# Performance work log

Hardware: AMD Instinct MI355X
Metric: run time of the kernel (lower is better)

Reference implementation:

```python
import jax, jax.numpy as jnp
import numpy as np

B, N, E = 4, 25000, 1600000
NODE_DIM, EMBED = 64, 64
NUM = B * N


def setup_inputs() -> dict:
    key = jax.random.key(0)
    ks = jax.random.split(key, 12)
    p = lambda k, s: jax.random.normal(k, s, jnp.float32) * 0.05
    z = lambda s: jnp.zeros(s, jnp.float32)
    return {
        "node_feat": jax.random.normal(ks[0], (B, N, NODE_DIM), jnp.float32),
        "src": jax.random.randint(ks[1], (E,), 0, NUM),
        "dst": jax.random.randint(ks[2], (E,), 0, NUM),
        "edge_weight": jax.random.uniform(ks[3], (E,), jnp.float32),
        "h": z((NUM, EMBED)),
        "W_cz": p(ks[4], (NODE_DIM, EMBED)), "b_cz": z((EMBED,)),
        "W_cr": p(ks[5], (NODE_DIM, EMBED)), "b_cr": z((EMBED,)),
        "W_ch": p(ks[6], (NODE_DIM, EMBED)), "b_ch": z((EMBED,)),
        "W_lz": p(ks[7], (2 * EMBED, EMBED)), "b_lz": z((EMBED,)),
        "W_lr": p(ks[8], (2 * EMBED, EMBED)), "b_lr": z((EMBED,)),
        "W_lh": p(ks[9], (2 * EMBED, EMBED)), "b_lh": z((EMBED,)),
        "W_head": p(ks[10], (EMBED, 1)), "b_head": z((1,)),
    }


def gcn_conv(x, W, b, src, dst, ew):
    # PyG GCNConv: self-loops (fill=1) + symmetric normalization, then linear.
    n = x.shape[0]
    loop = jnp.arange(n)
    s = jnp.concatenate([src, loop])
    d = jnp.concatenate([dst, loop])
    w = jnp.concatenate([ew, jnp.ones((n,), x.dtype)])
    deg = jax.ops.segment_sum(w, d, num_segments=n)
    dinv = jnp.where(deg > 0, jax.lax.rsqrt(deg), 0.0)
    norm = dinv[s] * w * dinv[d]                      # [E+n]
    xw = x @ W                                        # [n, EMBED]
    out = jax.ops.segment_sum(xw[s] * norm[:, None], d, num_segments=n)
    return out + b


def tgcn_cell(x, h, src, dst, ew,
              W_cz, b_cz, W_cr, b_cr, W_ch, b_ch,
              W_lz, b_lz, W_lr, b_lr, W_lh, b_lh):
    Z = jax.nn.sigmoid(
        jnp.concatenate([gcn_conv(x, W_cz, b_cz, src, dst, ew), h], axis=1) @ W_lz + b_lz)
    R = jax.nn.sigmoid(
        jnp.concatenate([gcn_conv(x, W_cr, b_cr, src, dst, ew), h], axis=1) @ W_lr + b_lr)
    H_tilde = jnp.tanh(
        jnp.concatenate([gcn_conv(x, W_ch, b_ch, src, dst, ew), h * R], axis=1) @ W_lh + b_lh)
    return Z * h + (1.0 - Z) * H_tilde


def reference(node_feat, src, dst, edge_weight, h,
              W_cz, b_cz, W_cr, b_cr, W_ch, b_ch,
              W_lz, b_lz, W_lr, b_lr, W_lh, b_lh,
              W_head, b_head):
    Bv, Nv, _ = node_feat.shape
    x = node_feat.reshape(Bv * Nv, -1)
    h0 = tgcn_cell(x, h, src, dst, edge_weight,
                   W_cz, b_cz, W_cr, b_cr, W_ch, b_ch,
                   W_lz, b_lz, W_lr, b_lr, W_lh, b_lh)
    z = jax.nn.relu(h0)
    z = (z @ W_head + b_head).reshape(Bv, Nv, -1)
    return (z, h0)
```

## Files before the change

kernel.cpp:

```cpp
#include <hip/hip_runtime.h>
#include <hip/hip_fp16.h>
#include <stdint.h>

typedef unsigned long long u64;
typedef _Float16 half8 __attribute__((ext_vector_type(8)));
typedef float f32x4 __attribute__((ext_vector_type(4)));

#define EPB 6144
#define CAPC 5440

__device__ __forceinline__ float sigm(float x) { return 1.0f / (1.0f + __expf(-x)); }
__device__ __forceinline__ float tanhfast(float x) { return 1.0f - 2.0f / (__expf(2.0f * x) + 1.0f); }
__device__ __forceinline__ int rli(int v, int k) { return __builtin_amdgcn_readlane(v, k); }
__device__ __forceinline__ float rlf(float v, int k) {
    return __int_as_float(__builtin_amdgcn_readlane(__float_as_int(v), k));
}

__global__ void k_pre(const float* __restrict__ Wcz, const float* __restrict__ bcz,
                      const float* __restrict__ Wcr, const float* __restrict__ bcr,
                      const float* __restrict__ Wch, const float* __restrict__ bch,
                      const float* __restrict__ Wlz, const float* __restrict__ blz,
                      const float* __restrict__ Wlr, const float* __restrict__ blr,
                      const float* __restrict__ Wlh, const float* __restrict__ blh,
                      const float4* __restrict__ h4, __half* __restrict__ aggh,
                      __half* __restrict__ B1f, __half* __restrict__ B2f,
                      float* __restrict__ bias, int* __restrict__ cursor, int hq) {
    int bid = blockIdx.x;
    if (bid < 113) {
        int tid = bid * 256 + threadIdx.x;
        if (tid < 1024) cursor[tid] = 0;
        if (tid < 24576) {
            int k = tid / 192, nc = tid % 192;
            int g = nc >> 6, j = nc & 63;
            const float* Wc = (g == 0) ? Wcz : (g == 1) ? Wcr : Wch;
            const float* Wl = (g == 0) ? Wlz : (g == 1) ? Wlr : Wlh;
            float v;
            if (k < 64) {
                float acc = 0.f;
                for (int m = 0; m < 64; m++) acc += Wc[k * 64 + m] * Wl[m * 64 + j];
                v = acc;
            } else {
                v = (g < 2) ? Wl[k * 64 + j] : 0.f;
            }
            int kt = k >> 5, nt = nc >> 4;
            int lane = (((k >> 3) & 3) << 4) | (nc & 15);
            B1f[(((kt * 12 + nt) * 64 + lane) << 3) + (k & 7)] = (__half)v;
        } else if (tid < 24576 + 4096) {
            int t = tid - 24576;
            int k = t >> 6, nc = t & 63;
            float v = Wlh[(64 + k) * 64 + nc];
            int kt = k >> 5, nt = nc >> 4;
            int lane = (((k >> 3) & 3) << 4) | (nc & 15);
            B2f[(((kt * 4 + nt) * 64 + lane) << 3) + (k & 7)] = (__half)v;
        } else if (tid < 24576 + 4096 + 192) {
            int t = tid - 24576 - 4096;
            int g = t >> 6, j = t & 63;
            const float* bc = (g == 0) ? bcz : (g == 1) ? bcr : bch;
            const float* Wl = (g == 0) ? Wlz : (g == 1) ? Wlr : Wlh;
            const float* bl = (g == 0) ? blz : (g == 1) ? blr : blh;
            float acc = bl[j];
            for (int m = 0; m < 64; m++) acc += bc[m] * Wl[m * 64 + j];
            bias[t] = acc;
        }
    } else {
        int i = (bid - 113) * 256 + threadIdx.x;
        if (i < hq) {
            float4 hv = h4[i];
            int elem = i * 4;
            int node = elem >> 6, c = elem & 63;
            __half2* ho = (__half2*)(aggh + (((size_t)node) << 7) + 64 + c);
            ho[0] = __floats2half2_rn(hv.x, hv.y);
            ho[1] = __floats2half2_rn(hv.z, hv.w);
        }
    }
}

__global__ void __launch_bounds__(1024) k_bin(const int* __restrict__ src, const int* __restrict__ dst,
                                              const float* __restrict__ ew,
                                              int* __restrict__ cursor, u64* __restrict__ binned,
                                              int E, int R) {
    __shared__ u64 recs[EPB];
    __shared__ int hist[512];
    __shared__ int loff[512];
    __shared__ int curL[512];
    __shared__ int gbase[512];

    int tid = threadIdx.x;
    if (tid < 512) hist[tid] = 0;
    __syncthreads();

    int base = blockIdx.x * EPB;
    int cntE = min(EPB, E - base);

    u64 myrec[6];
    int myr[6];
#pragma unroll
    for (int j = 0; j < 6; j++) {
        int idx = tid + j * 1024;
        if (idx < cntE) {
            int e = base + idx;
            int d = dst[e], s = src[e];
            float w = ew[e];
            int r = d >> 8;
            myr[j] = r;
            myrec[j] = (u64)((unsigned)s | ((unsigned)(d & 255) << 17)) | ((u64)__float_as_uint(w) << 32);
            atomicAdd(&hist[r], 1);
        } else myr[j] = -1;
    }
    __syncthreads();

    if (tid < 64) {
        int sums[8], tot = 0;
#pragma unroll
        for (int q = 0; q < 8; q++) { sums[q] = hist[tid * 8 + q]; tot += sums[q]; }
        int scan = tot;
#pragma unroll
        for (int o = 1; o < 64; o <<= 1) {
            int v = __shfl_up(scan, o);
            if (tid >= o) scan += v;
        }
        int run = scan - tot;
#pragma unroll
        for (int q = 0; q < 8; q++) { loff[tid * 8 + q] = run; run += sums[q]; }
    }
    if (tid < 512) curL[tid] = 0;
    if (tid < R) {
        int hcnt = hist[tid];
        if (hcnt > 0) gbase[tid] = tid * CAPC + atomicAdd(&cursor[tid], hcnt);
    }
    __syncthreads();

#pragma unroll
    for (int j = 0; j < 6; j++) {
        if (myr[j] >= 0) {
            int p = atomicAdd(&curL[myr[j]], 1);
            recs[loff[myr[j]] + p] = myrec[j];
        }
    }
    __syncthreads();

    int wave = tid >> 6, lane = tid & 63;
    for (int r = wave; r < R; r += 16) {
        int len = hist[r];
        if (!len) continue;
        int gb = gbase[r], lo = loff[r];
        int capEnd = (r + 1) * CAPC;
        for (int i = lane; i < len; i += 64)
            if (gb + i < capEnd) binned[(size_t)(gb + i)] = recs[lo + i];
    }
}

__global__ void __launch_bounds__(1024) k_sort(const int* __restrict__ cursor,
                                               u64* __restrict__ binned,
                                               const float2* __restrict__ x2,
                                               float* __restrict__ dinv,
                                               __half2* __restrict__ xs2,
                                               int* __restrict__ off_g, int* __restrict__ len_g,
                                               int n) {
    __shared__ u64 srt[CAPC];
    __shared__ int hist[256];
    __shared__ int noff[256];
    __shared__ int cur[256];
    __shared__ float degw[256];

    int r = blockIdx.x, tid = threadIdx.x;
    if (tid < 256) { hist[tid] = 0; degw[tid] = 0.f; }
    __syncthreads();

    int cnt = min(cursor[r], CAPC);
    u64* B = binned + (size_t)r * CAPC;

    for (int i = tid; i < cnt; i += 1024) {
        u64 m = B[i];
        int dl = ((unsigned)m >> 17) & 255;
        atomicAdd(&hist[dl], 1);
        atomicAdd(&degw[dl], __uint_as_float((unsigned)(m >> 32)));
    }
    __syncthreads();

    if (tid < 64) {
        int s0 = hist[tid * 4], s1 = hist[tid * 4 + 1], s2 = hist[tid * 4 + 2], s3 = hist[tid * 4 + 3];
        int tot = s0 + s1 + s2 + s3;
        int scan = tot;
#pragma unroll
        for (int o = 1; o < 64; o <<= 1) {
            int v = __shfl_up(scan, o);
            if (tid >= o) scan += v;
        }
        int run = scan - tot;
        noff[tid * 4] = run; run += s0;
        noff[tid * 4 + 1] = run; run += s1;
        noff[tid * 4 + 2] = run; run += s2;
        noff[tid * 4 + 3] = run;
    }
    __syncthreads();

    if (tid < 256) {
        int node = r * 256 + tid;
        float dv = rsqrtf(1.0f + degw[tid]);
        if (node < n) {
            dinv[node] = dv;
            off_g[node] = r * CAPC + noff[tid];
            len_g[node] = hist[tid];
        }
        cur[tid] = noff[tid];
        degw[tid] = dv;
    }
    __syncthreads();

    for (int i = tid; i < cnt; i += 1024) {
        u64 m = B[i];
        int dl = ((unsigned)m >> 17) & 255;
        int p = atomicAdd(&cur[dl], 1);
        srt[p] = (u64)((unsigned)m & 0x1FFFF) | (m & 0xFFFFFFFF00000000ULL);
    }
    __syncthreads();

    for (int i = tid; i < cnt; i += 1024) B[i] = srt[i];
    int nbase = r * 256;
    for (int i = tid; i < 256 * 32; i += 1024) {
        int nl = i >> 5, cp = i & 31;
        int node = nbase + nl;
        if (node < n) {
            float2 xv = x2[((size_t)node << 5) + cp];
            float dv = degw[nl];
            xs2[((size_t)node << 5) + cp] = __floats2half2_rn(dv * xv.x, dv * xv.y);
        }
    }
}

__global__ void __launch_bounds__(256) k_gather(const int* __restrict__ off_g, const int* __restrict__ len_g,
                                                const u64* __restrict__ csr, const float* __restrict__ dinv,
                                                const __half* __restrict__ xs,
                                                __half* __restrict__ aggh, int n) {
    int lane = threadIdx.x & 63;
    int wid = __builtin_amdgcn_readfirstlane(threadIdx.x >> 6);
    int d = blockIdx.x * 4 + wid;
    if (d >= n) return;
    int o0 = off_g[d], L = len_g[d];
    float dd = dinv[d];
    float acc[16];
#pragma unroll
    for (int j = 0; j < 16; j++) acc[j] = 0.f;
    acc[0] = (float)xs[((size_t)d << 6) + lane];

    for (int base = 0; base < L; base += 64) {
        int c = min(64, L - base);
        u64 m = (lane < c) ? csr[(size_t)(o0 + base) + lane] : 0;
        int s_l = (unsigned)m & 0x1FFFF;
        float w_l = __uint_as_float((unsigned)(m >> 32));
        int k = 0;
        for (; k + 16 <= c; k += 16) {
            int ss[16]; float ww[16], xr[16];
#pragma unroll
            for (int j = 0; j < 16; j++) { ss[j] = rli(s_l, k + j); ww[j] = rlf(w_l, k + j); }
#pragma unroll
            for (int j = 0; j < 16; j++) xr[j] = (float)xs[((size_t)ss[j] << 6) + lane];
#pragma unroll
            for (int j = 0; j < 16; j++) acc[j] = fmaf(ww[j], xr[j], acc[j]);
        }
        for (; k + 4 <= c; k += 4) {
            int ss[4]; float ww[4], xr[4];
#pragma unroll
            for (int j = 0; j < 4; j++) { ss[j] = rli(s_l, k + j); ww[j] = rlf(w_l, k + j); }
#pragma unroll
            for (int j = 0; j < 4; j++) xr[j] = (float)xs[((size_t)ss[j] << 6) + lane];
#pragma unroll
            for (int j = 0; j < 4; j++) acc[j] = fmaf(ww[j], xr[j], acc[j]);
        }
        for (; k < c; k++) {
            int s0 = rli(s_l, k);
            float w0 = rlf(w_l, k);
            acc[0] = fmaf(w0, (float)xs[((size_t)s0 << 6) + lane], acc[0]);
        }
    }
    float s = ((acc[0] + acc[1]) + (acc[2] + acc[3])) + ((acc[4] + acc[5]) + (acc[6] + acc[7]))
            + ((acc[8] + acc[9]) + (acc[10] + acc[11])) + ((acc[12] + acc[13]) + (acc[14] + acc[15]));
    aggh[((size_t)d << 7) + lane] = (__half)(dd * s);
}

__global__ void __launch_bounds__(256, 2) k_node(
        const __half* __restrict__ aggh,
        const __half* __restrict__ B1f_g, const __half* __restrict__ B2f_g,
        const float* __restrict__ bias_g, const float* __restrict__ Whead,
        const float* __restrict__ bhead,
        float* __restrict__ out_head, float* __restrict__ out_h, int n) {

    __shared__ __half B1s[24576];
    __shared__ __half B2s[4096];
    __shared__ float biasS[192];
    __shared__ float whS[64];
    __shared__ __half hrb[4][16 * 72];

    int tid = threadIdx.x;
    {
        const uint4* s1 = (const uint4*)B1f_g; uint4* d1 = (uint4*)B1s;
        for (int i = tid; i < 3072; i += 256) d1[i] = s1[i];
        const uint4* s2 = (const uint4*)B2f_g; uint4* d2 = (uint4*)B2s;
        for (int i = tid; i < 512; i += 256) d2[i] = s2[i];
        if (tid < 192) biasS[tid] = bias_g[tid];
        if (tid < 64) whS[tid] = Whead[tid];
    }
    __syncthreads();

    int lane = tid & 63;
    int wave = tid >> 6;
    int quad = lane >> 4;
    int l15 = lane & 15;

    float bz4[4], br4[4], bh4[4], wh4[4];
#pragma unroll
    for (int nt = 0; nt < 4; nt++) {
        bz4[nt] = biasS[nt * 16 + l15];
        br4[nt] = biasS[64 + nt * 16 + l15];
        bh4[nt] = biasS[128 + nt * 16 + l15];
        wh4[nt] = whS[nt * 16 + l15];
    }
    float bhv = bhead[0];
    __half* myhr = &hrb[wave][0];
    const half8* B1v = (const half8*)B1s;
    const half8* B2v = (const half8*)B2s;

    int mbase = blockIdx.x * 64 + wave * 16;
    if (mbase < n) {
        const half8* arow = (const half8*)(aggh + (((size_t)(mbase + l15)) << 7) + (quad << 3));
        half8 a0 = arow[0], a1 = arow[4], a2 = arow[8], a3 = arow[12];

        f32x4 acc[12];
#pragma unroll
        for (int nt = 0; nt < 12; nt++) acc[nt] = (f32x4){0.f, 0.f, 0.f, 0.f};

#pragma unroll
        for (int nt = 0; nt < 12; nt++) {
            acc[nt] = __builtin_amdgcn_mfma_f32_16x16x32_f16(a0, B1v[(0 * 12 + nt) * 64 + lane], acc[nt], 0, 0, 0);
            acc[nt] = __builtin_amdgcn_mfma_f32_16x16x32_f16(a1, B1v[(1 * 12 + nt) * 64 + lane], acc[nt], 0, 0, 0);
            acc[nt] = __builtin_amdgcn_mfma_f32_16x16x32_f16(a2, B1v[(2 * 12 + nt) * 64 + lane], acc[nt], 0, 0, 0);
            acc[nt] = __builtin_amdgcn_mfma_f32_16x16x32_f16(a3, B1v[(3 * 12 + nt) * 64 + lane], acc[nt], 0, 0, 0);
        }

        float hv[4][4];
#pragma unroll
        for (int nt = 0; nt < 4; nt++)
#pragma unroll
            for (int r = 0; r < 4; r++)
                hv[nt][r] = (float)aggh[(((size_t)(mbase + quad * 4 + r)) << 7) + 64 + nt * 16 + l15];

        float Z[4][4];
#pragma unroll
        for (int nt = 0; nt < 4; nt++)
#pragma unroll
            for (int r = 0; r < 4; r++) {
                Z[nt][r] = sigm(acc[nt][r] + bz4[nt]);
                float R = sigm(acc[4 + nt][r] + br4[nt]);
                myhr[(quad * 4 + r) * 72 + nt * 16 + l15] = (__half)(hv[nt][r] * R);
            }
        __builtin_amdgcn_s_waitcnt(0);

        half8 a2f0 = *(const half8*)(myhr + l15 * 72 + quad * 8);
        half8 a2f1 = *(const half8*)(myhr + l15 * 72 + 32 + quad * 8);

#pragma unroll
        for (int nt = 0; nt < 4; nt++) {
            acc[8 + nt] = __builtin_amdgcn_mfma_f32_16x16x32_f16(a2f0, B2v[(0 * 4 + nt) * 64 + lane], acc[8 + nt], 0, 0, 0);
            acc[8 + nt] = __builtin_amdgcn_mfma_f32_16x16x32_f16(a2f1, B2v[(1 * 4 + nt) * 64 + lane], acc[8 + nt], 0, 0, 0);
        }

        float pr0 = 0.f, pr1 = 0.f, pr2 = 0.f, pr3 = 0.f;
#pragma unroll
        for (int nt = 0; nt < 4; nt++) {
#pragma unroll
            for (int r = 0; r < 4; r++) {
                float Ht = tanhfast(acc[8 + nt][r] + bh4[nt]);
                float z = Z[nt][r];
                float hn = z * hv[nt][r] + (1.f - z) * Ht;
                out_h[((size_t)(mbase + quad * 4 + r)) * 64 + nt * 16 + l15] = hn;
                float rv = fmaxf(hn, 0.f) * wh4[nt];
                if (r == 0) pr0 += rv; else if (r == 1) pr1 += rv; else if (r == 2) pr2 += rv; else pr3 += rv;
            }
        }
#pragma unroll
        for (int o = 1; o < 16; o <<= 1) {
            pr0 += __shfl_xor(pr0, o);
            pr1 += __shfl_xor(pr1, o);
            pr2 += __shfl_xor(pr2, o);
            pr3 += __shfl_xor(pr3, o);
        }
        if (l15 == 0) {
            out_head[mbase + quad * 4 + 0] = pr0 + bhv;
            out_head[mbase + quad * 4 + 1] = pr1 + bhv;
            out_head[mbase + quad * 4 + 2] = pr2 + bhv;
            out_head[mbase + quad * 4 + 3] = pr3 + bhv;
        }
    }
}

extern "C" void kernel_launch(void* const* d_in, const int* in_sizes, int n_in,
                              void* d_out, int out_size, void* d_ws, size_t ws_size,
                              hipStream_t stream) {
    const float* x     = (const float*)d_in[0];
    const int*   src   = (const int*)d_in[1];
    const int*   dst   = (const int*)d_in[2];
    const float* ew    = (const float*)d_in[3];
    const float* h     = (const float*)d_in[4];
    const float* Wcz   = (const float*)d_in[5];
    const float* bcz   = (const float*)d_in[6];
    const float* Wcr   = (const float*)d_in[7];
    const float* bcr   = (const float*)d_in[8];
    const float* Wch   = (const float*)d_in[9];
    const float* bch   = (const float*)d_in[10];
    const float* Wlz   = (const float*)d_in[11];
    const float* blz   = (const float*)d_in[12];
    const float* Wlr   = (const float*)d_in[13];
    const float* blr   = (const float*)d_in[14];
    const float* Wlh   = (const float*)d_in[15];
    const float* blh   = (const float*)d_in[16];
    const float* Whead = (const float*)d_in[17];
    const float* bhead = (const float*)d_in[18];

    int E = in_sizes[1];
    int n = in_sizes[4] / 64;
    int R = (n + 255) >> 8;

    __half* aggh = (__half*)d_ws;
    __half* xs   = aggh + (size_t)n * 128;
    u64*   binned = (u64*)(xs + (size_t)n * 64);
    float* dinv  = (float*)(binned + (size_t)R * CAPC);
    int*   off_g = (int*)(dinv + n);
    int*   len_g = off_g + n;
    int*   cursor = len_g + n;
    __half* B1f  = (__half*)(cursor + 1024);
    __half* B2f  = B1f + 24576;
    float* bias  = (float*)(B2f + 4096);

    float* out_head = (float*)d_out;
    float* out_h    = out_head + n;

    int hq = n * 16;
    int nbB = (E + EPB - 1) / EPB;
    int gridPre = 113 + (hq + 255) / 256;

    k_pre<<<gridPre, 256, 0, stream>>>(Wcz, bcz, Wcr, bcr, Wch, bch,
                                       Wlz, blz, Wlr, blr, Wlh, blh,
                                       (const float4*)h, aggh, B1f, B2f, bias, cursor, hq);
    k_bin<<<nbB, 1024, 0, stream>>>(src, dst, ew, cursor, binned, E, R);
    k_sort<<<R, 1024, 0, stream>>>(cursor, binned, (const float2*)x, dinv,
                                   (__half2*)xs, off_g, len_g, n);
    k_gather<<<(n + 3) / 4, 256, 0, stream>>>(off_g, len_g, binned, dinv, xs, aggh, n);
    k_node<<<(n + 63) / 64, 256, 0, stream>>>(aggh, B1f, B2f, bias, Whead, bhead,
                                              out_head, out_h, n);
}
```

Baseline: 245.9 us.

## Fuse edge gather into node GRU kernel and read h directly

Merges the per-destination gather into the node MFMA kernel: each wave aggregates its 16 nodes into LDS and then runs the gate matmuls, which removes the aggh intermediate round-trip and one launch. The h state is now read and converted from fp32 inside the node kernel instead of in the pre-kernel, and weights are read from global memory instead of being staged in LDS. The risk is lower gather parallelism, since each wave processes 16 nodes serially, and more global weight reads.

```diff
diff --git a/kernel.cpp b/kernel.cpp
--- a/kernel.cpp
+++ b/kernel.cpp
@@ -22,56 +22,42 @@
                       const float* __restrict__ Wlz, const float* __restrict__ blz,
                       const float* __restrict__ Wlr, const float* __restrict__ blr,
                       const float* __restrict__ Wlh, const float* __restrict__ blh,
-                      const float4* __restrict__ h4, __half* __restrict__ aggh,
                       __half* __restrict__ B1f, __half* __restrict__ B2f,
-                      float* __restrict__ bias, int* __restrict__ cursor, int hq) {
-    int bid = blockIdx.x;
-    if (bid < 113) {
-        int tid = bid * 256 + threadIdx.x;
-        if (tid < 1024) cursor[tid] = 0;
-        if (tid < 24576) {
-            int k = tid / 192, nc = tid % 192;
-            int g = nc >> 6, j = nc & 63;
-            const float* Wc = (g == 0) ? Wcz : (g == 1) ? Wcr : Wch;
-            const float* Wl = (g == 0) ? Wlz : (g == 1) ? Wlr : Wlh;
-            float v;
-            if (k < 64) {
-                float acc = 0.f;
-                for (int m = 0; m < 64; m++) acc += Wc[k * 64 + m] * Wl[m * 64 + j];
-                v = acc;
-            } else {
-                v = (g < 2) ? Wl[k * 64 + j] : 0.f;
-            }
-            int kt = k >> 5, nt = nc >> 4;
-            int lane = (((k >> 3) & 3) << 4) | (nc & 15);
-            B1f[(((kt * 12 + nt) * 64 + lane) << 3) + (k & 7)] = (__half)v;
-        } else if (tid < 24576 + 4096) {
-            int t = tid - 24576;
-            int k = t >> 6, nc = t & 63;
-            float v = Wlh[(64 + k) * 64 + nc];
-            int kt = k >> 5, nt = nc >> 4;
-            int lane = (((k >> 3) & 3) << 4) | (nc & 15);
-            B2f[(((kt * 4 + nt) * 64 + lane) << 3) + (k & 7)] = (__half)v;
-        } else if (tid < 24576 + 4096 + 192) {
-            int t = tid - 24576 - 4096;
-            int g = t >> 6, j = t & 63;
-            const float* bc = (g == 0) ? bcz : (g == 1) ? bcr : bch;
-            const float* Wl = (g == 0) ? Wlz : (g == 1) ? Wlr : Wlh;
-            const float* bl = (g == 0) ? blz : (g == 1) ? blr : blh;
-            float acc = bl[j];
-            for (int m = 0; m < 64; m++) acc += bc[m] * Wl[m * 64 + j];
-            bias[t] = acc;
-        }
-    } else {
-        int i = (bid - 113) * 256 + threadIdx.x;
-        if (i < hq) {
-            float4 hv = h4[i];
-            int elem = i * 4;
-            int node = elem >> 6, c = elem & 63;
-            __half2* ho = (__half2*)(aggh + (((size_t)node) << 7) + 64 + c);
-            ho[0] = __floats2half2_rn(hv.x, hv.y);
-            ho[1] = __floats2half2_rn(hv.z, hv.w);
-        }
+                      float* __restrict__ bias, int* __restrict__ cursor) {
+    int tid = blockIdx.x * 256 + threadIdx.x;
+    if (tid < 1024) cursor[tid] = 0;
+    if (tid < 24576) {
+        int k = tid / 192, nc = tid % 192;
+        int g = nc >> 6, j = nc & 63;
+        const float* Wc = (g == 0) ? Wcz : (g == 1) ? Wcr : Wch;
+        const float* Wl = (g == 0) ? Wlz : (g == 1) ? Wlr : Wlh;
+        float v;
+        if (k < 64) {
+            float acc = 0.f;
+            for (int m = 0; m < 64; m++) acc += Wc[k * 64 + m] * Wl[m * 64 + j];
+            v = acc;
+        } else {
+            v = (g < 2) ? Wl[k * 64 + j] : 0.f;
+        }
+        int kt = k >> 5, nt = nc >> 4;
+        int lane = (((k >> 3) & 3) << 4) | (nc & 15);
+        B1f[(((kt * 12 + nt) * 64 + lane) << 3) + (k & 7)] = (__half)v;
+    } else if (tid < 24576 + 4096) {
+        int t = tid - 24576;
+        int k = t >> 6, nc = t & 63;
+        float v = Wlh[(64 + k) * 64 + nc];
+        int kt = k >> 5, nt = nc >> 4;
+        int lane = (((k >> 3) & 3) << 4) | (nc & 15);
+        B2f[(((kt * 4 + nt) * 64 + lane) << 3) + (k & 7)] = (__half)v;
+    } else if (tid < 24576 + 4096 + 192) {
+        int t = tid - 24576 - 4096;
+        int g = t >> 6, j = t & 63;
+        const float* bc = (g == 0) ? bcz : (g == 1) ? bcr : bch;
+        const float* Wl = (g == 0) ? Wlz : (g == 1) ? Wlr : Wlh;
+        const float* bl = (g == 0) ? blz : (g == 1) ? blr : blh;
+        float acc = bl[j];
+        for (int m = 0; m < 64; m++) acc += bc[m] * Wl[m * 64 + j];
+        bias[t] = acc;
     }
 }
 
@@ -229,168 +215,155 @@
     }
 }
 
-__global__ void __launch_bounds__(256) k_gather(const int* __restrict__ off_g, const int* __restrict__ len_g,
-                                                const u64* __restrict__ csr, const float* __restrict__ dinv,
-                                                const __half* __restrict__ xs,
-                                                __half* __restrict__ aggh, int n) {
-    int lane = threadIdx.x & 63;
-    int wid = __builtin_amdgcn_readfirstlane(threadIdx.x >> 6);
-    int d = blockIdx.x * 4 + wid;
-    if (d >= n) return;
-    int o0 = off_g[d], L = len_g[d];
-    float dd = dinv[d];
-    float acc[16];
-#pragma unroll
-    for (int j = 0; j < 16; j++) acc[j] = 0.f;
-    acc[0] = (float)xs[((size_t)d << 6) + lane];
-
-    for (int base = 0; base < L; base += 64) {
-        int c = min(64, L - base);
-        u64 m = (lane < c) ? csr[(size_t)(o0 + base) + lane] : 0;
-        int s_l = (unsigned)m & 0x1FFFF;
-        float w_l = __uint_as_float((unsigned)(m >> 32));
-        int k = 0;
-        for (; k + 16 <= c; k += 16) {
-            int ss[16]; float ww[16], xr[16];
-#pragma unroll
-            for (int j = 0; j < 16; j++) { ss[j] = rli(s_l, k + j); ww[j] = rlf(w_l, k + j); }
-#pragma unroll
-            for (int j = 0; j < 16; j++) xr[j] = (float)xs[((size_t)ss[j] << 6) + lane];
-#pragma unroll
-            for (int j = 0; j < 16; j++) acc[j] = fmaf(ww[j], xr[j], acc[j]);
-        }
-        for (; k + 4 <= c; k += 4) {
-            int ss[4]; float ww[4], xr[4];
-#pragma unroll
-            for (int j = 0; j < 4; j++) { ss[j] = rli(s_l, k + j); ww[j] = rlf(w_l, k + j); }
-#pragma unroll
-            for (int j = 0; j < 4; j++) xr[j] = (float)xs[((size_t)ss[j] << 6) + lane];
-#pragma unroll
-            for (int j = 0; j < 4; j++) acc[j] = fmaf(ww[j], xr[j], acc[j]);
-        }
-        for (; k < c; k++) {
-            int s0 = rli(s_l, k);
-            float w0 = rlf(w_l, k);
-            acc[0] = fmaf(w0, (float)xs[((size_t)s0 << 6) + lane], acc[0]);
-        }
-    }
-    float s = ((acc[0] + acc[1]) + (acc[2] + acc[3])) + ((acc[4] + acc[5]) + (acc[6] + acc[7]))
-            + ((acc[8] + acc[9]) + (acc[10] + acc[11])) + ((acc[12] + acc[13]) + (acc[14] + acc[15]));
-    aggh[((size_t)d << 7) + lane] = (__half)(dd * s);
-}
-
-__global__ void __launch_bounds__(256, 2) k_node(
-        const __half* __restrict__ aggh,
+__global__ void __launch_bounds__(256, 2) k_gnode(
+        const int* __restrict__ off_g, const int* __restrict__ len_g,
+        const u64* __restrict__ csr, const float* __restrict__ dinv,
+        const __half* __restrict__ xs, const float* __restrict__ hglob,
         const __half* __restrict__ B1f_g, const __half* __restrict__ B2f_g,
         const float* __restrict__ bias_g, const float* __restrict__ Whead,
         const float* __restrict__ bhead,
         float* __restrict__ out_head, float* __restrict__ out_h, int n) {
 
-    __shared__ __half B1s[24576];
-    __shared__ __half B2s[4096];
-    __shared__ float biasS[192];
-    __shared__ float whS[64];
-    __shared__ __half hrb[4][16 * 72];
+    __shared__ __half buf[4][16 * 72];
 
     int tid = threadIdx.x;
-    {
-        const uint4* s1 = (const uint4*)B1f_g; uint4* d1 = (uint4*)B1s;
-        for (int i = tid; i < 3072; i += 256) d1[i] = s1[i];
-        const uint4* s2 = (const uint4*)B2f_g; uint4* d2 = (uint4*)B2s;
-        for (int i = tid; i < 512; i += 256) d2[i] = s2[i];
-        if (tid < 192) biasS[tid] = bias_g[tid];
-        if (tid < 64) whS[tid] = Whead[tid];
-    }
-    __syncthreads();
-
     int lane = tid & 63;
-    int wave = tid >> 6;
+    int wave = __builtin_amdgcn_readfirstlane(tid >> 6);
     int quad = lane >> 4;
     int l15 = lane & 15;
 
+    int mb = blockIdx.x * 64 + wave * 16;
+    if (mb >= n) return;
+    __half* myb = &buf[wave][0];
+
+    for (int t = 0; t < 16; t++) {
+        int d = mb + t;
+        int o0 = off_g[d], L = len_g[d];
+        float dd = dinv[d];
+        float acc[16];
+#pragma unroll
+        for (int j = 0; j < 16; j++) acc[j] = 0.f;
+        acc[0] = (float)xs[((size_t)d << 6) + lane];
+        for (int base = 0; base < L; base += 64) {
+            int c = min(64, L - base);
+            u64 m = (lane < c) ? csr[(size_t)(o0 + base) + lane] : 0;
+            int s_l = (unsigned)m & 0x1FFFF;
+            float w_l = __uint_as_float((unsigned)(m >> 32));
+            int k = 0;
+            for (; k + 16 <= c; k += 16) {
+                int ss[16]; float ww[16], xr[16];
+#pragma unroll
+                for (int j = 0; j < 16; j++) { ss[j] = rli(s_l, k + j); ww[j] = rlf(w_l, k + j); }
+#pragma unroll
+                for (int j = 0; j < 16; j++) xr[j] = (float)xs[((size_t)ss[j] << 6) + lane];
+#pragma unroll
+                for (int j = 0; j < 16; j++) acc[j] = fmaf(ww[j], xr[j], acc[j]);
+            }
+            for (; k + 4 <= c; k += 4) {
+                int ss[4]; float ww[4], xr[4];
+#pragma unroll
+                for (int j = 0; j < 4; j++) { ss[j] = rli(s_l, k + j); ww[j] = rlf(w_l, k + j); }
+#pragma unroll
+                for (int j = 0; j < 4; j++) xr[j] = (float)xs[((size_t)ss[j] << 6) + lane];
+#pragma unroll
+                for (int j = 0; j < 4; j++) acc[j] = fmaf(ww[j], xr[j], acc[j]);
+            }
+            for (; k < c; k++) {
+                int s0 = rli(s_l, k);
+                float w0 = rlf(w_l, k);
+                acc[0] = fmaf(w0, (float)xs[((size_t)s0 << 6) + lane], acc[0]);
+            }
+        }
+        float s = ((acc[0] + acc[1]) + (acc[2] + acc[3])) + ((acc[4] + acc[5]) + (acc[6] + acc[7]))
+                + ((acc[8] + acc[9]) + (acc[10] + acc[11])) + ((acc[12] + acc[13]) + (acc[14] + acc[15]));
+        myb[t * 72 + lane] = (__half)(dd * s);
+    }
+    __builtin_amdgcn_s_waitcnt(0);
+
+    half8 a0 = *(const half8*)(myb + l15 * 72 + quad * 8);
+    half8 a1 = *(const half8*)(myb + l15 * 72 + 32 + quad * 8);
+    const float* hrow = hglob + (size_t)(mb + l15) * 64 + quad * 8;
+    half8 a2, a3;
+#pragma unroll
+    for (int j = 0; j < 8; j++) a2[j] = (_Float16)hrow[j];
+#pragma unroll
+    for (int j = 0; j < 8; j++) a3[j] = (_Float16)hrow[32 + j];
+
+    const half8* B1v = (const half8*)B1f_g;
+    const half8* B2v = (const half8*)B2f_g;
+    f32x4 acc12[12];
+#pragma unroll
+    for (int nt = 0; nt < 12; nt++) acc12[nt] = (f32x4){0.f, 0.f, 0.f, 0.f};
+#pragma unroll
+    for (int nt = 0; nt < 12; nt++) {
+        acc12[nt] = __builtin_amdgcn_mfma_f32_16x16x32_f16(a0, B1v[(0 * 12 + nt) * 64 + lane], acc12[nt], 0, 0, 0);
+        acc12[nt] = __builtin_amdgcn_mfma_f32_16x16x32_f16(a1, B1v[(1 * 12 + nt) * 64 + lane], acc12[nt], 0, 0, 0);
+        acc12[nt] = __builtin_amdgcn_mfma_f32_16x16x32_f16(a2, B1v[(2 * 12 + nt) * 64 + lane], acc12[nt], 0, 0, 0);
+        acc12[nt] = __builtin_amdgcn_mfma_f32_16x16x32_f16(a3, B1v[(3 * 12 + nt) * 64 + lane], acc12[nt], 0, 0, 0);
+    }
+
     float bz4[4], br4[4], bh4[4], wh4[4];
 #pragma unroll
     for (int nt = 0; nt < 4; nt++) {
-        bz4[nt] = biasS[nt * 16 + l15];
-        br4[nt] = biasS[64 + nt * 16 + l15];
-        bh4[nt] = biasS[128 + nt * 16 + l15];
-        wh4[nt] = whS[nt * 16 + l15];
+        bz4[nt] = bias_g[nt * 16 + l15];
+        br4[nt] = bias_g[64 + nt * 16 + l15];
+        bh4[nt] = bias_g[128 + nt * 16 + l15];
+        wh4[nt] = Whead[nt * 16 + l15];
     }
     float bhv = bhead[0];
-    __half* myhr = &hrb[wave][0];
-    const half8* B1v = (const half8*)B1s;
-    const half8* B2v = (const half8*)B2s;
-
-    int mbase = blockIdx.x * 64 + wave * 16;
-    if (mbase < n) {
-        const half8* arow = (const half8*)(aggh + (((size_t)(mbase + l15)) << 7) + (quad << 3));
-        half8 a0 = arow[0], a1 = arow[4], a2 = arow[8], a3 = arow[12];
-
-        f32x4 acc[12];
-#pragma unroll
-        for (int nt = 0; nt < 12; nt++) acc[nt] = (f32x4){0.f, 0.f, 0.f, 0.f};
-
-#pragma unroll
-        for (int nt = 0; nt < 12; nt++) {
-            acc[nt] = __builtin_amdgcn_mfma_f32_16x16x32_f16(a0, B1v[(0 * 12 + nt) * 64 + lane], acc[nt], 0, 0, 0);
-            acc[nt] = __builtin_amdgcn_mfma_f32_16x16x32_f16(a1, B1v[(1 * 12 + nt) * 64 + lane], acc[nt], 0, 0, 0);
-            acc[nt] = __builtin_amdgcn_mfma_f32_16x16x32_f16(a2, B1v[(2 * 12 + nt) * 64 + lane], acc[nt], 0, 0, 0);
-            acc[nt] = __builtin_amdgcn_mfma_f32_16x16x32_f16(a3, B1v[(3 * 12 + nt) * 64 + lane], acc[nt], 0, 0, 0);
-        }
-
-        float hv[4][4];
-#pragma unroll
-        for (int nt = 0; nt < 4; nt++)
-#pragma unroll
-            for (int r = 0; r < 4; r++)
-                hv[nt][r] = (float)aggh[(((size_t)(mbase + quad * 4 + r)) << 7) + 64 + nt * 16 + l15];
-
-        float Z[4][4];
-#pragma unroll
-        for (int nt = 0; nt < 4; nt++)
-#pragma unroll
-            for (int r = 0; r < 4; r++) {
-                Z[nt][r] = sigm(acc[nt][r] + bz4[nt]);
-                float R = sigm(acc[4 + nt][r] + br4[nt]);
-                myhr[(quad * 4 + r) * 72 + nt * 16 + l15] = (__half)(hv[nt][r] * R);
-            }
-        __builtin_amdgcn_s_waitcnt(0);
-
-        half8 a2f0 = *(const half8*)(myhr + l15 * 72 + quad * 8);
-        half8 a2f1 = *(const half8*)(myhr + l15 * 72 + 32 + quad * 8);
-
-#pragma unroll
-        for (int nt = 0; nt < 4; nt++) {
-            acc[8 + nt] = __builtin_amdgcn_mfma_f32_16x16x32_f16(a2f0, B2v[(0 * 4 + nt) * 64 + lane], acc[8 + nt], 0, 0, 0);
-            acc[8 + nt] = __builtin_amdgcn_mfma_f32_16x16x32_f16(a2f1, B2v[(1 * 4 + nt) * 64 + lane], acc[8 + nt], 0, 0, 0);
-        }
-
-        float pr0 = 0.f, pr1 = 0.f, pr2 = 0.f, pr3 = 0.f;
-#pragma unroll
-        for (int nt = 0; nt < 4; nt++) {
-#pragma unroll
-            for (int r = 0; r < 4; r++) {
-                float Ht = tanhfast(acc[8 + nt][r] + bh4[nt]);
-                float z = Z[nt][r];
-                float hn = z * hv[nt][r] + (1.f - z) * Ht;
-                out_h[((size_t)(mbase + quad * 4 + r)) * 64 + nt * 16 + l15] = hn;
-                float rv = fmaxf(hn, 0.f) * wh4[nt];
-                if (r == 0) pr0 += rv; else if (r == 1) pr1 += rv; else if (r == 2) pr2 += rv; else pr3 += rv;
-            }
-        }
-#pragma unroll
-        for (int o = 1; o < 16; o <<= 1) {
-            pr0 += __shfl_xor(pr0, o);
-            pr1 += __shfl_xor(pr1, o);
-            pr2 += __shfl_xor(pr2, o);
-            pr3 += __shfl_xor(pr3, o);
-        }
-        if (l15 == 0) {
-            out_head[mbase + quad * 4 + 0] = pr0 + bhv;
-            out_head[mbase + quad * 4 + 1] = pr1 + bhv;
-            out_head[mbase + quad * 4 + 2] = pr2 + bhv;
-            out_head[mbase + quad * 4 + 3] = pr3 + bhv;
-        }
+
+    float hv[4][4];
+#pragma unroll
+    for (int nt = 0; nt < 4; nt++)
+#pragma unroll
+        for (int r = 0; r < 4; r++)
+            hv[nt][r] = hglob[(size_t)(mb + quad * 4 + r) * 64 + nt * 16 + l15];
+
+    float Z[4][4];
+#pragma unroll
+    for (int nt = 0; nt < 4; nt++)
+#pragma unroll
+        for (int r = 0; r < 4; r++) {
+            Z[nt][r] = sigm(acc12[nt][r] + bz4[nt]);
+            float R = sigm(acc12[4 + nt][r] + br4[nt]);
+            myb[(quad * 4 + r) * 72 + nt * 16 + l15] = (__half)(hv[nt][r] * R);
+        }
+    __builtin_amdgcn_s_waitcnt(0);
+
+    half8 a2f0 = *(const half8*)(myb + l15 * 72 + quad * 8);
+    half8 a2f1 = *(const half8*)(myb + l15 * 72 + 32 + quad * 8);
+
+#pragma unroll
+    for (int nt = 0; nt < 4; nt++) {
+        acc12[8 + nt] = __builtin_amdgcn_mfma_f32_16x16x32_f16(a2f0, B2v[(0 * 4 + nt) * 64 + lane], acc12[8 + nt], 0, 0, 0);
+        acc12[8 + nt] = __builtin_amdgcn_mfma_f32_16x16x32_f16(a2f1, B2v[(1 * 4 + nt) * 64 + lane], acc12[8 + nt], 0, 0, 0);
+    }
+
+    float pr0 = 0.f, pr1 = 0.f, pr2 = 0.f, pr3 = 0.f;
+#pragma unroll
+    for (int nt = 0; nt < 4; nt++) {
+#pragma unroll
+        for (int r = 0; r < 4; r++) {
+            float Ht = tanhfast(acc12[8 + nt][r] + bh4[nt]);
+            float z = Z[nt][r];
+            float hn = z * hv[nt][r] + (1.f - z) * Ht;
+            out_h[(size_t)(mb + quad * 4 + r) * 64 + nt * 16 + l15] = hn;
+            float rv = fmaxf(hn, 0.f) * wh4[nt];
+            if (r == 0) pr0 += rv; else if (r == 1) pr1 += rv; else if (r == 2) pr2 += rv; else pr3 += rv;
+        }
+    }
+#pragma unroll
+    for (int o = 1; o < 16; o <<= 1) {
+        pr0 += __shfl_xor(pr0, o);
+        pr1 += __shfl_xor(pr1, o);
+        pr2 += __shfl_xor(pr2, o);
+        pr3 += __shfl_xor(pr3, o);
+    }
+    if (l15 == 0) {
+        out_head[mb + quad * 4 + 0] = pr0 + bhv;
+        out_head[mb + quad * 4 + 1] = pr1 + bhv;
+        out_head[mb + quad * 4 + 2] = pr2 + bhv;
+        out_head[mb + quad * 4 + 3] = pr3 + bhv;
     }
 }
 
@@ -421,8 +394,7 @@
     int n = in_sizes[4] / 64;
     int R = (n + 255) >> 8;
 
-    __half* aggh = (__half*)d_ws;
-    __half* xs   = aggh + (size_t)n * 128;
+    __half* xs   = (__half*)d_ws;
     u64*   binned = (u64*)(xs + (size_t)n * 64);
     float* dinv  = (float*)(binned + (size_t)R * CAPC);
     int*   off_g = (int*)(dinv + n);
@@ -435,17 +407,14 @@
     float* out_head = (float*)d_out;
     float* out_h    = out_head + n;
 
-    int hq = n * 16;
     int nbB = (E + EPB - 1) / EPB;
-    int gridPre = 113 + (hq + 255) / 256;
-
-    k_pre<<<gridPre, 256, 0, stream>>>(Wcz, bcz, Wcr, bcr, Wch, bch,
-                                       Wlz, blz, Wlr, blr, Wlh, blh,
-                                       (const float4*)h, aggh, B1f, B2f, bias, cursor, hq);
+
+    k_pre<<<113, 256, 0, stream>>>(Wcz, bcz, Wcr, bcr, Wch, bch,
+                                   Wlz, blz, Wlr, blr, Wlh, blh, B1f, B2f, bias, cursor);
     k_bin<<<nbB, 1024, 0, stream>>>(src, dst, ew, cursor, binned, E, R);
     k_sort<<<R, 1024, 0, stream>>>(cursor, binned, (const float2*)x, dinv,
                                    (__half2*)xs, off_g, len_g, n);
-    k_gather<<<(n + 3) / 4, 256, 0, stream>>>(off_g, len_g, binned, dinv, xs, aggh, n);
-    k_node<<<(n + 63) / 64, 256, 0, stream>>>(aggh, B1f, B2f, bias, Whead, bhead,
-                                              out_head, out_h, n);
-}
+    k_gnode<<<(n + 63) / 64, 256, 0, stream>>>(off_g, len_g, binned, dinv, xs, h,
+                                               B1f, B2f, bias, Whead, bhead,
+                                               out_head, out_h, n);
+}
```

New measurement: 267.3 us. 8.7% more time.
